# Kernel tuning notes

Measured on AMD Instinct MI355X. Metric: run time of the kernel, lower is better.

The kernel has to match this reference:

```python
import jax, jax.numpy as jnp
import numpy as np

D_MODEL = 384
NUM_CODES = 256
BETAS = (0.05, 0.25, 0.6)
B = 8192


def _vq(x, codebook, beta):
    """Standard EMA-VQ forward: nearest-code lookup + straight-through + commitment loss.
    x: (B, N, D), codebook: (K, D).
    (EMA buffer updates are training-time, no-grad side effects and are omitted.)"""
    flat = x.reshape(-1, x.shape[-1])  # (B*N, D)
    d2 = (jnp.sum(flat * flat, axis=-1, keepdims=True)
          - 2.0 * flat @ codebook.T
          + jnp.sum(codebook * codebook, axis=-1))  # (B*N, K)
    idx = jnp.argmin(d2, axis=-1)                    # (B*N,)
    q_hard = codebook[idx].reshape(x.shape)          # gather (B, N, D)
    idx = idx.reshape(x.shape[:-1])                  # (B, N)
    loss = beta * jnp.mean(jnp.square(jax.lax.stop_gradient(q_hard) - x))
    q = x + jax.lax.stop_gradient(q_hard - x)        # straight-through estimator
    return q, loss, idx


def setup_inputs() -> dict:
    key = jax.random.key(0)
    k0, k1, k2, k3, k4, k5 = jax.random.split(key, 6)
    return {
        "l0_feats": jax.random.normal(k0, (B, 4, D_MODEL), dtype=jnp.float32),
        "l1_feats": jax.random.normal(k1, (B, 16, D_MODEL), dtype=jnp.float32),
        "l2_feats": jax.random.normal(k2, (B, 16, D_MODEL), dtype=jnp.float32),
        "codebook0": jax.random.normal(k3, (NUM_CODES, D_MODEL), dtype=jnp.float32),
        "codebook1": jax.random.normal(k4, (NUM_CODES, D_MODEL), dtype=jnp.float32),
        "codebook2": jax.random.normal(k5, (NUM_CODES, D_MODEL), dtype=jnp.float32),
    }


def reference(l0_feats, l1_feats, l2_feats, codebook0, codebook1, codebook2):
    q0, loss0, idx0 = _vq(l0_feats, codebook0, BETAS[0])
    q1, loss1, idx1 = _vq(l1_feats, codebook1, BETAS[1])
    q2, loss2, idx2 = _vq(l2_feats, codebook2, BETAS[2])
    total_vq_loss = loss0 + loss1 + loss2
    return (idx0, idx1, idx2, total_vq_loss, q0, q1, q2)
```

## Files before the change

kernel.cpp:

```cpp
#include <hip/hip_runtime.h>


typedef _Float16 half8 __attribute__((ext_vector_type(8)));
typedef float f32x16 __attribute__((ext_vector_type(16)));

#define D_MODEL 384
#define NSEG 96
#define NKT 12
#define BM 64
#define RTAU 0.5f

__device__ __forceinline__ float4 ld4(const float* p) { return *(const float4*)p; }

__device__ __forceinline__ half8 cvt8h(const float4& a, const float4& b) {
  half8 h;
  h[0] = (_Float16)a.x; h[1] = (_Float16)a.y; h[2] = (_Float16)a.z; h[3] = (_Float16)a.w;
  h[4] = (_Float16)b.x; h[5] = (_Float16)b.y; h[6] = (_Float16)b.z; h[7] = (_Float16)b.w;
  return h;
}

__device__ __forceinline__ void gload_lds16(const void* g, void* l) {
  __builtin_amdgcn_global_load_lds(
      (const __attribute__((address_space(1))) unsigned int*)g,
      (__attribute__((address_space(3))) unsigned int*)l, 16, 0, 0);
}

__global__ __launch_bounds__(64) void vq_norms(const float* __restrict__ c0,
                                               const float* __restrict__ c1,
                                               const float* __restrict__ c2,
                                               float* __restrict__ en,
                                               int* __restrict__ counts) {
  if (blockIdx.x == 0 && threadIdx.x < 4) counts[threadIdx.x] = 0;
  const int row = blockIdx.x;
  const float* cb = (row < 256) ? c0 : ((row < 512) ? c1 : c2);
  const int n = row & 255;
  const int lane = threadIdx.x;
  const float* r = cb + (size_t)n * D_MODEL;
  float s = 0.f;
  for (int c = lane; c < D_MODEL; c += 64) s = fmaf(r[c], r[c], s);
  for (int m = 1; m < 64; m <<= 1) s += __shfl_xor(s, m, 64);
  if (lane == 0) en[row] = s;
}

__global__ __launch_bounds__(256) void vq_split_cb(const float* __restrict__ c0,
                                                   const float* __restrict__ c1,
                                                   const float* __restrict__ c2,
                                                   half8* __restrict__ bh) {
  const int t = blockIdx.x * 256 + threadIdx.x;
  const int lvl = t / 12288;
  const int rem = t - lvl * 12288;
  const int kt = rem >> 10;
  const int f = (rem >> 6) & 15;
  const int lane = rem & 63;
  const int code = (f >> 1) * 32 + (lane & 31);
  const int k0 = kt * 32 + (f & 1) * 16 + (lane >> 5) * 8;
  const float* cb = (lvl == 0) ? c0 : ((lvl == 1) ? c1 : c2);
  const float4 a = ld4(cb + code * D_MODEL + k0);
  const float4 b = ld4(cb + code * D_MODEL + k0 + 4);
  bh[t] = cvt8h(a, b);
}

__global__ __launch_bounds__(256, 3) void vq_mfma_all(
    const float* __restrict__ l0, const float* __restrict__ l1,
    const float* __restrict__ l2, const float* __restrict__ c0,
    const float* __restrict__ c1, const float* __restrict__ c2,
    const float* __restrict__ en_all,
    const half8* __restrict__ bh_pre,
    float* __restrict__ out, float* __restrict__ dmin_all,
    float* __restrict__ xn_all,
    int* __restrict__ list0, int* __restrict__ list1, int* __restrict__ list2,
    int* __restrict__ counts) {
  __shared__ __align__(16) unsigned char smem[40960];
  float*  scanbuf = (float*)smem;
  float4* red     = (float4*)(smem + 32768);
  float*  en_s    = (float*)(smem + 36864);
  float4* rowres  = (float4*)(smem + 37888);
  float*  xns     = (float*)(smem + 38912);
  int*    idxs    = (int*)(smem + 39168);

  const int swz = (blockIdx.x & 7) * 576 + (blockIdx.x >> 3);
  int lvl, blk;
  if (swz < 512)       { lvl = 0; blk = swz; }
  else if (swz < 2560) { lvl = 1; blk = swz - 512; }
  else                 { lvl = 2; blk = swz - 2560; }
  const float* x  = (lvl == 0) ? l0 : ((lvl == 1) ? l1 : l2);
  const float* cb = (lvl == 0) ? c0 : ((lvl == 1) ? c1 : c2);
  const float* en = en_all + lvl * 256;
  const half8* bh = bh_pre + lvl * 12288;
  const long ioff = (lvl == 0) ? 0 : ((lvl == 1) ? 32768 : 163840);
  float* out_idx = out + ioff;
  float* out_q   = out + ((lvl == 0) ? 294913L : ((lvl == 1) ? 12877825L : 63209473L));
  float* dmin_lvl = dmin_all + ioff;
  float* xn_lvl   = xn_all + ioff;
  int* list = (lvl == 0) ? list0 : ((lvl == 1) ? list1 : list2);
  int* cnt  = counts + lvl;

  const int tid = threadIdx.x;
  const int lane = tid & 63;
  const int w = tid >> 6, wm = w >> 1, wn = w & 1;
  const int c31 = lane & 31, h = lane >> 5;
  const long m0 = (long)blk * BM;

  const float* ap = x + (m0 + wm * 32 + c31) * (long)D_MODEL + h * 8;

  f32x16 acc[4];
#pragma unroll
  for (int n = 0; n < 4; ++n)
#pragma unroll
    for (int i = 0; i < 16; ++i) acc[n][i] = 0.f;

  float xn_part = 0.f;

  float4 ra0 = ld4(ap + 0), ra1 = ld4(ap + 4), ra2 = ld4(ap + 16), ra3 = ld4(ap + 20);
#pragma unroll
  for (int r = 0; r < 4; ++r) {
    const int f = r * 4 + w;
    gload_lds16(bh + (size_t)(f * 64 + lane), (void*)(smem + f * 1024));
  }
  xn_part = fmaf(ra0.x, ra0.x, xn_part); xn_part = fmaf(ra0.y, ra0.y, xn_part);
  xn_part = fmaf(ra0.z, ra0.z, xn_part); xn_part = fmaf(ra0.w, ra0.w, xn_part);
  xn_part = fmaf(ra1.x, ra1.x, xn_part); xn_part = fmaf(ra1.y, ra1.y, xn_part);
  xn_part = fmaf(ra1.z, ra1.z, xn_part); xn_part = fmaf(ra1.w, ra1.w, xn_part);
  xn_part = fmaf(ra2.x, ra2.x, xn_part); xn_part = fmaf(ra2.y, ra2.y, xn_part);
  xn_part = fmaf(ra2.z, ra2.z, xn_part); xn_part = fmaf(ra2.w, ra2.w, xn_part);
  xn_part = fmaf(ra3.x, ra3.x, xn_part); xn_part = fmaf(ra3.y, ra3.y, xn_part);
  xn_part = fmaf(ra3.z, ra3.z, xn_part); xn_part = fmaf(ra3.w, ra3.w, xn_part);
  half8 ahc0 = cvt8h(ra0, ra1);
  half8 ahc1 = cvt8h(ra2, ra3);
  __syncthreads();

#pragma unroll
  for (int kt = 0; kt < NKT; ++kt) {
    const int cur = kt & 1;
    const int nxt = cur ^ 1;
    float4 rb0, rb1, rb2, rb3;
    if (kt + 1 < NKT) {
#pragma unroll
      for (int r = 0; r < 4; ++r) {
        const int f = r * 4 + w;
        gload_lds16(bh + (size_t)(kt + 1) * 1024 + (size_t)(f * 64 + lane),
                    (void*)(smem + nxt * 16384 + f * 1024));
      }
      const int ko = (kt + 1) * 32;
      rb0 = ld4(ap + ko); rb1 = ld4(ap + ko + 4);
      rb2 = ld4(ap + ko + 16); rb3 = ld4(ap + ko + 20);
    }
    {
      const half8* Bh = (const half8*)(smem + cur * 16384);
#pragma unroll
      for (int n = 0; n < 4; ++n) {
        const int nt = wn * 4 + n;
        half8 b0 = Bh[(nt * 2 + 0) * 64 + lane];
        half8 b1 = Bh[(nt * 2 + 1) * 64 + lane];
        acc[n] = __builtin_amdgcn_mfma_f32_32x32x16_f16(ahc0, b0, acc[n], 0, 0, 0);
        acc[n] = __builtin_amdgcn_mfma_f32_32x32x16_f16(ahc1, b1, acc[n], 0, 0, 0);
      }
    }
    if (kt + 1 < NKT) {
      xn_part = fmaf(rb0.x, rb0.x, xn_part); xn_part = fmaf(rb0.y, rb0.y, xn_part);
      xn_part = fmaf(rb0.z, rb0.z, xn_part); xn_part = fmaf(rb0.w, rb0.w, xn_part);
      xn_part = fmaf(rb1.x, rb1.x, xn_part); xn_part = fmaf(rb1.y, rb1.y, xn_part);
      xn_part = fmaf(rb1.z, rb1.z, xn_part); xn_part = fmaf(rb1.w, rb1.w, xn_part);
      xn_part = fmaf(rb2.x, rb2.x, xn_part); xn_part = fmaf(rb2.y, rb2.y, xn_part);
      xn_part = fmaf(rb2.z, rb2.z, xn_part); xn_part = fmaf(rb2.w, rb2.w, xn_part);
      xn_part = fmaf(rb3.x, rb3.x, xn_part); xn_part = fmaf(rb3.y, rb3.y, xn_part);
      xn_part = fmaf(rb3.z, rb3.z, xn_part); xn_part = fmaf(rb3.w, rb3.w, xn_part);
      ahc0 = cvt8h(rb0, rb1);
      ahc1 = cvt8h(rb2, rb3);
      __syncthreads();
    }
  }

  {
    const float xr = xn_part + __shfl_xor(xn_part, 32, 64);
    if (wn == 0 && lane < 32) xns[wm * 32 + lane] = xr;
  }
  en_s[tid] = en[tid];

#pragma unroll 1
  for (int b = 0; b < 2; ++b) {
    __syncthreads();
    if (wm == b) {
#pragma unroll
      for (int n = 0; n < 4; ++n) {
        const int colbase = wn * 128 + n * 32 + c31;
#pragma unroll
        for (int rr = 0; rr < 16; ++rr) {
          const int row_b = (rr & 3) + ((rr >> 2) << 3) + (h << 2);
          const int p = colbase ^ ((row_b & 3) << 3);
          scanbuf[row_b * 256 + p] = fmaf(-2.f, acc[n][rr], en_s[colbase]);
        }
      }
    }
    __syncthreads();
    {
      const int srow = tid >> 3, chunk = tid & 7;
      float b1 = 1e30f, b2 = 1e30f; int i1 = 0, i2 = 0;
#pragma unroll
      for (int u = 0; u < 32; ++u) {
        const int col = chunk + u * 8;
        const float d = scanbuf[srow * 256 + (col ^ ((srow & 3) << 3))];
        if (d < b1) { b2 = b1; i2 = i1; b1 = d; i1 = col; }
        else if (d < b2) { b2 = d; i2 = col; }
      }
      red[srow * 8 + chunk] = make_float4(b1, __int_as_float(i1), b2, __int_as_float(i2));
    }
    __syncthreads();
    if (tid < 32) {
      float4 q = red[tid * 8 + 0];
      float fb1 = q.x, fb2 = q.z;
      int fi1 = __float_as_int(q.y), fi2 = __float_as_int(q.w);
#pragma unroll
      for (int c = 1; c < 8; ++c) {
        q = red[tid * 8 + c];
        const float c1 = q.x, c2 = q.z;
        const int j1 = __float_as_int(q.y), j2 = __float_as_int(q.w);
        if (c1 < fb1 || (c1 == fb1 && j1 < fi1)) {
          if (fb1 < c2 || (fb1 == c2 && fi1 < j2)) { fb2 = fb1; fi2 = fi1; }
          else { fb2 = c2; fi2 = j2; }
          fb1 = c1; fi1 = j1;
        } else if (c1 < fb2 || (c1 == fb2 && j1 < fi2)) { fb2 = c1; fi2 = j1; }
      }
      rowres[b * 32 + tid] = make_float4(fb1, __int_as_float(fi1), fb2, __int_as_float(fi2));
    }
  }
  __syncthreads();

  if (tid < BM) {
    const int m = tid;
    const float4 qv = rowres[m];
    const float fb1 = qv.x, fb2 = qv.z;
    const int fi1 = __float_as_int(qv.y);
    const float xn = xns[m];
    idxs[m] = fi1;
    out_idx[m0 + m] = (float)fi1;
    dmin_lvl[m0 + m] = xn + fb1;
    xn_lvl[m0 + m] = xn;
    const bool flg = (fb2 - fb1 < RTAU);
    const unsigned long long mask = __ballot(flg);
    const int nf = __popcll(mask);
    int base = 0;
    if (tid == 0 && nf) base = atomicAdd(cnt, nf);
    base = __shfl(base, 0, 64);
    if (flg) {
      const int pos = __popcll(mask & ((1ull << tid) - 1ull));
      list[base + pos] = (int)(m0 + m);
    }
  }
  __syncthreads();

  float* qb = out_q + m0 * (long)D_MODEL;
  for (int g = tid; g < BM * NSEG; g += 256) {
    const int m = g / NSEG;
    const int seg = g - m * NSEG;
    *(float4*)(qb + m * (long)D_MODEL + seg * 4) = ld4(cb + (long)idxs[m] * D_MODEL + seg * 4);
  }
}

__global__ __launch_bounds__(256) void vq_rescue_all(
    const float* __restrict__ l0, const float* __restrict__ l1,
    const float* __restrict__ l2, const float* __restrict__ c0,
    const float* __restrict__ c1, const float* __restrict__ c2,
    const float* __restrict__ en_all,
    const int* __restrict__ list0, const int* __restrict__ list1,
    const int* __restrict__ list2, const int* __restrict__ counts,
    float* __restrict__ out, float* __restrict__ dmin_all,
    const float* __restrict__ xn_all) {
  __shared__ float xs[8][D_MODEL];
  __shared__ double dall[8][256];
  __shared__ int rows_s[8];
  __shared__ float xns_s[8];
  __shared__ int best_s[8];

  const int lvl = blockIdx.x >> 7;
  const int sb  = blockIdx.x & 127;
  const float* x  = (lvl == 0) ? l0 : ((lvl == 1) ? l1 : l2);
  const float* cb = (lvl == 0) ? c0 : ((lvl == 1) ? c1 : c2);
  const int* list = (lvl == 0) ? list0 : ((lvl == 1) ? list1 : list2);
  const long ioff = (lvl == 0) ? 0 : ((lvl == 1) ? 32768 : 163840);
  float* out_idx = out + ioff;
  float* out_q   = out + ((lvl == 0) ? 294913L : ((lvl == 1) ? 12877825L : 63209473L));
  float* dmin_lvl = dmin_all + ioff;
  const float* xn_lvl = xn_all + ioff;

  const int tid = threadIdx.x;
  const int count = counts[lvl];
  const int nch = (count + 7) >> 3;
  const int w = tid >> 6, lane = tid & 63;
  const float* crow = cb + (long)tid * D_MODEL;

  for (int c = sb; c < nch; c += 128) {
    const int base = c << 3;
    const int R = min(8, count - base);
    if (tid < 8) {
      const int j = min(tid, R - 1);
      const int r = list[base + j];
      rows_s[tid] = r;
      xns_s[tid] = xn_lvl[r];
    }
    __syncthreads();
#pragma unroll
    for (int r = 0; r < 8; ++r)
      if (tid < NSEG) *(float4*)&xs[r][tid * 4] = ld4(x + (long)rows_s[r] * D_MODEL + tid * 4);
    __syncthreads();

    double en_d = 0.0;
    double dot[8] = {0.0, 0.0, 0.0, 0.0, 0.0, 0.0, 0.0, 0.0};
    for (int k = 0; k < D_MODEL; ++k) {
      const double cd = (double)crow[k];
      en_d = fma(cd, cd, en_d);
#pragma unroll
      for (int r = 0; r < 8; ++r)
        dot[r] = fma(cd, (double)xs[r][k], dot[r]);
    }
#pragma unroll
    for (int r = 0; r < 8; ++r)
      dall[r][tid] = fma(-2.0, dot[r], en_d);
    __syncthreads();

#pragma unroll
    for (int rr = 0; rr < 2; ++rr) {
      const int r = w + rr * 4;
      if (r < R) {
        double best = dall[r][lane]; int bidx = lane;
#pragma unroll
        for (int u = 1; u < 4; ++u) {
          const int code = lane + u * 64;
          const double d = dall[r][code];
          if (d < best) { best = d; bidx = code; }
        }
        for (int mm = 1; mm < 64; mm <<= 1) {
          const double ov = __shfl_xor(best, mm, 64);
          const int oi = __shfl_xor(bidx, mm, 64);
          if (ov < best || (ov == best && oi < bidx)) { best = ov; bidx = oi; }
        }
        if (lane == 0) {
          const int row = rows_s[r];
          out_idx[row] = (float)bidx;
          dmin_lvl[row] = xns_s[r] + (float)best;
          best_s[r] = bidx;
        }
      }
    }
    __syncthreads();
#pragma unroll
    for (int r = 0; r < 8; ++r)
      if (r < R && tid < NSEG)
        *(float4*)(out_q + (long)rows_s[r] * D_MODEL + tid * 4) =
            ld4(cb + (long)best_s[r] * D_MODEL + tid * 4);
    __syncthreads();
  }
}

__global__ __launch_bounds__(256) void loss_stage1(const float* __restrict__ dmin,
                                                   double* __restrict__ lp) {
  const int b = blockIdx.x;
  const int tid = threadIdx.x;
  const long r0 = (long)b * 512;
  __shared__ double sh[256];
  sh[tid] = (double)dmin[r0 + tid] + (double)dmin[r0 + 256 + tid];
  __syncthreads();
  for (int st = 128; st > 0; st >>= 1) {
    if (tid < st) sh[tid] += sh[tid + st];
    __syncthreads();
  }
  if (tid == 0) {
    double scale;
    if (b < 64)       scale = 0.05 / (32768.0 * 384.0);
    else if (b < 320) scale = 0.25 / (131072.0 * 384.0);
    else              scale = 0.60 / (131072.0 * 384.0);
    lp[b] = sh[0] * scale;
  }
}

__global__ __launch_bounds__(256) void loss_stage2(const double* __restrict__ lp,
                                                   float* __restrict__ out_loss) {
  const int tid = threadIdx.x;
  __shared__ double sh[256];
  sh[tid] = lp[tid] + lp[tid + 256] + ((tid < 64) ? lp[tid + 512] : 0.0);
  __syncthreads();
  for (int st = 128; st > 0; st >>= 1) {
    if (tid < st) sh[tid] += sh[tid + st];
    __syncthreads();
  }
  if (tid == 0) out_loss[0] = (float)sh[0];
}

extern "C" void kernel_launch(void* const* d_in, const int* in_sizes, int n_in,
                              void* d_out, int out_size, void* d_ws, size_t ws_size,
                              hipStream_t stream) {
  const float* l0 = (const float*)d_in[0];
  const float* l1 = (const float*)d_in[1];
  const float* l2 = (const float*)d_in[2];
  const float* c0 = (const float*)d_in[3];
  const float* c1 = (const float*)d_in[4];
  const float* c2 = (const float*)d_in[5];
  float* out = (float*)d_out;

  float* wsf = (float*)d_ws;
  int*   counts   = (int*)wsf;
  float* en       = wsf + 4;
  float* dmin_all = wsf + 772;
  float* xn_all   = wsf + 295684;
  int*   list0    = (int*)(wsf + 590596);
  int*   list1    = (int*)(wsf + 623364);
  int*   list2    = (int*)(wsf + 754436);
  double* lp      = (double*)(wsf + 885508);
  half8* bh_pre   = (half8*)(wsf + 886660);

  vq_norms<<<768, 64, 0, stream>>>(c0, c1, c2, en, counts);
  vq_split_cb<<<144, 256, 0, stream>>>(c0, c1, c2, bh_pre);

  vq_mfma_all<<<4608, 256, 0, stream>>>(l0, l1, l2, c0, c1, c2, en,
                                        bh_pre, out,
                                        dmin_all, xn_all,
                                        list0, list1, list2, counts);

  vq_rescue_all<<<384, 256, 0, stream>>>(l0, l1, l2, c0, c1, c2, en,
                                         list0, list1, list2, counts,
                                         out, dmin_all, xn_all);

  loss_stage1<<<576, 256, 0, stream>>>(dmin_all, lp);
  loss_stage2<<<1, 256, 0, stream>>>(lp, out + 294912);
}
```

Baseline: 482.0 us.

## Read codebook fragments from global directly in MFMA loop, widen rescue grid

The MFMA distance kernel no longer stages the pre-split fp16 codebook tiles through LDS with async global-to-LDS loads and per-step barriers. Each wave now loads its B fragments straight from global memory (mostly L2-resident, since the codebook is small) into registers, which removes the double-buffered LDS pipeline and the per-k-tile __syncthreads. The rescue kernel grid grows from 128 to 1024 blocks per level so more chunks of ambiguous rows run in parallel. In exchange, B fragments are loaded redundantly by each wave instead of shared through LDS, and global load latency is exposed in the MFMA loop.

Result: slower. 526.2 us (+9.2%).

```diff
diff --git a/kernel.cpp b/kernel.cpp
--- a/kernel.cpp
+++ b/kernel.cpp
@@ -17,12 +17,6 @@
   h[0] = (_Float16)a.x; h[1] = (_Float16)a.y; h[2] = (_Float16)a.z; h[3] = (_Float16)a.w;
   h[4] = (_Float16)b.x; h[5] = (_Float16)b.y; h[6] = (_Float16)b.z; h[7] = (_Float16)b.w;
   return h;
-}
-
-__device__ __forceinline__ void gload_lds16(const void* g, void* l) {
-  __builtin_amdgcn_global_load_lds(
-      (const __attribute__((address_space(1))) unsigned int*)g,
-      (__attribute__((address_space(3))) unsigned int*)l, 16, 0, 0);
 }
 
 __global__ __launch_bounds__(64) void vq_norms(const float* __restrict__ c0,
@@ -59,6 +53,16 @@
   const float4 b = ld4(cb + code * D_MODEL + k0 + 4);
   bh[t] = cvt8h(a, b);
 }
+
+#define XN8(v0, v1, v2, v3)                                                     \
+  xn_part = fmaf(v0.x, v0.x, xn_part); xn_part = fmaf(v0.y, v0.y, xn_part);     \
+  xn_part = fmaf(v0.z, v0.z, xn_part); xn_part = fmaf(v0.w, v0.w, xn_part);     \
+  xn_part = fmaf(v1.x, v1.x, xn_part); xn_part = fmaf(v1.y, v1.y, xn_part);     \
+  xn_part = fmaf(v1.z, v1.z, xn_part); xn_part = fmaf(v1.w, v1.w, xn_part);     \
+  xn_part = fmaf(v2.x, v2.x, xn_part); xn_part = fmaf(v2.y, v2.y, xn_part);     \
+  xn_part = fmaf(v2.z, v2.z, xn_part); xn_part = fmaf(v2.w, v2.w, xn_part);     \
+  xn_part = fmaf(v3.x, v3.x, xn_part); xn_part = fmaf(v3.y, v3.y, xn_part);     \
+  xn_part = fmaf(v3.z, v3.z, xn_part); xn_part = fmaf(v3.w, v3.w, xn_part);
 
 __global__ __launch_bounds__(256, 3) void vq_mfma_all(
     const float* __restrict__ l0, const float* __restrict__ l1,
@@ -102,6 +106,7 @@
   const long m0 = (long)blk * BM;
 
   const float* ap = x + (m0 + wm * 32 + c31) * (long)D_MODEL + h * 8;
+  const half8* bhw = bh + wn * 512 + lane;
 
   f32x16 acc[4];
 #pragma unroll
@@ -112,62 +117,37 @@
   float xn_part = 0.f;
 
   float4 ra0 = ld4(ap + 0), ra1 = ld4(ap + 4), ra2 = ld4(ap + 16), ra3 = ld4(ap + 20);
-#pragma unroll
-  for (int r = 0; r < 4; ++r) {
-    const int f = r * 4 + w;
-    gload_lds16(bh + (size_t)(f * 64 + lane), (void*)(smem + f * 1024));
-  }
-  xn_part = fmaf(ra0.x, ra0.x, xn_part); xn_part = fmaf(ra0.y, ra0.y, xn_part);
-  xn_part = fmaf(ra0.z, ra0.z, xn_part); xn_part = fmaf(ra0.w, ra0.w, xn_part);
-  xn_part = fmaf(ra1.x, ra1.x, xn_part); xn_part = fmaf(ra1.y, ra1.y, xn_part);
-  xn_part = fmaf(ra1.z, ra1.z, xn_part); xn_part = fmaf(ra1.w, ra1.w, xn_part);
-  xn_part = fmaf(ra2.x, ra2.x, xn_part); xn_part = fmaf(ra2.y, ra2.y, xn_part);
-  xn_part = fmaf(ra2.z, ra2.z, xn_part); xn_part = fmaf(ra2.w, ra2.w, xn_part);
-  xn_part = fmaf(ra3.x, ra3.x, xn_part); xn_part = fmaf(ra3.y, ra3.y, xn_part);
-  xn_part = fmaf(ra3.z, ra3.z, xn_part); xn_part = fmaf(ra3.w, ra3.w, xn_part);
+  XN8(ra0, ra1, ra2, ra3)
   half8 ahc0 = cvt8h(ra0, ra1);
   half8 ahc1 = cvt8h(ra2, ra3);
-  __syncthreads();
 
 #pragma unroll
   for (int kt = 0; kt < NKT; ++kt) {
-    const int cur = kt & 1;
-    const int nxt = cur ^ 1;
-    float4 rb0, rb1, rb2, rb3;
+    half8 b0 = bhw[kt * 1024 + 0 * 64];
+    half8 b1 = bhw[kt * 1024 + 1 * 64];
+    half8 b2 = bhw[kt * 1024 + 2 * 64];
+    half8 b3 = bhw[kt * 1024 + 3 * 64];
+    half8 b4 = bhw[kt * 1024 + 4 * 64];
+    half8 b5 = bhw[kt * 1024 + 5 * 64];
+    half8 b6 = bhw[kt * 1024 + 6 * 64];
+    half8 b7 = bhw[kt * 1024 + 7 * 64];
     if (kt + 1 < NKT) {
-#pragma unroll
-      for (int r = 0; r < 4; ++r) {
-        const int f = r * 4 + w;
-        gload_lds16(bh + (size_t)(kt + 1) * 1024 + (size_t)(f * 64 + lane),
-                    (void*)(smem + nxt * 16384 + f * 1024));
-      }
       const int ko = (kt + 1) * 32;
-      rb0 = ld4(ap + ko); rb1 = ld4(ap + ko + 4);
-      rb2 = ld4(ap + ko + 16); rb3 = ld4(ap + ko + 20);
-    }
-    {
-      const half8* Bh = (const half8*)(smem + cur * 16384);
-#pragma unroll
-      for (int n = 0; n < 4; ++n) {
-        const int nt = wn * 4 + n;
-        half8 b0 = Bh[(nt * 2 + 0) * 64 + lane];
-        half8 b1 = Bh[(nt * 2 + 1) * 64 + lane];
-        acc[n] = __builtin_amdgcn_mfma_f32_32x32x16_f16(ahc0, b0, acc[n], 0, 0, 0);
-        acc[n] = __builtin_amdgcn_mfma_f32_32x32x16_f16(ahc1, b1, acc[n], 0, 0, 0);
-      }
-    }
+      ra0 = ld4(ap + ko);      ra1 = ld4(ap + ko + 4);
+      ra2 = ld4(ap + ko + 16); ra3 = ld4(ap + ko + 20);
+    }
+    acc[0] = __builtin_amdgcn_mfma_f32_32x32x16_f16(ahc0, b0, acc[0], 0, 0, 0);
+    acc[0] = __builtin_amdgcn_mfma_f32_32x32x16_f16(ahc1, b1, acc[0], 0, 0, 0);
+    acc[1] = __builtin_amdgcn_mfma_f32_32x32x16_f16(ahc0, b2, acc[1], 0, 0, 0);
+    acc[1] = __builtin_amdgcn_mfma_f32_32x32x16_f16(ahc1, b3, acc[1], 0, 0, 0);
+    acc[2] = __builtin_amdgcn_mfma_f32_32x32x16_f16(ahc0, b4, acc[2], 0, 0, 0);
+    acc[2] = __builtin_amdgcn_mfma_f32_32x32x16_f16(ahc1, b5, acc[2], 0, 0, 0);
+    acc[3] = __builtin_amdgcn_mfma_f32_32x32x16_f16(ahc0, b6, acc[3], 0, 0, 0);
+    acc[3] = __builtin_amdgcn_mfma_f32_32x32x16_f16(ahc1, b7, acc[3], 0, 0, 0);
     if (kt + 1 < NKT) {
-      xn_part = fmaf(rb0.x, rb0.x, xn_part); xn_part = fmaf(rb0.y, rb0.y, xn_part);
-      xn_part = fmaf(rb0.z, rb0.z, xn_part); xn_part = fmaf(rb0.w, rb0.w, xn_part);
-      xn_part = fmaf(rb1.x, rb1.x, xn_part); xn_part = fmaf(rb1.y, rb1.y, xn_part);
-      xn_part = fmaf(rb1.z, rb1.z, xn_part); xn_part = fmaf(rb1.w, rb1.w, xn_part);
-      xn_part = fmaf(rb2.x, rb2.x, xn_part); xn_part = fmaf(rb2.y, rb2.y, xn_part);
-      xn_part = fmaf(rb2.z, rb2.z, xn_part); xn_part = fmaf(rb2.w, rb2.w, xn_part);
-      xn_part = fmaf(rb3.x, rb3.x, xn_part); xn_part = fmaf(rb3.y, rb3.y, xn_part);
-      xn_part = fmaf(rb3.z, rb3.z, xn_part); xn_part = fmaf(rb3.w, rb3.w, xn_part);
-      ahc0 = cvt8h(rb0, rb1);
-      ahc1 = cvt8h(rb2, rb3);
-      __syncthreads();
+      XN8(ra0, ra1, ra2, ra3)
+      ahc0 = cvt8h(ra0, ra1);
+      ahc1 = cvt8h(ra2, ra3);
     }
   }
 
@@ -272,8 +252,8 @@
   __shared__ float xns_s[8];
   __shared__ int best_s[8];
 
-  const int lvl = blockIdx.x >> 7;
-  const int sb  = blockIdx.x & 127;
+  const int lvl = blockIdx.x >> 10;
+  const int sb  = blockIdx.x & 1023;
   const float* x  = (lvl == 0) ? l0 : ((lvl == 1) ? l1 : l2);
   const float* cb = (lvl == 0) ? c0 : ((lvl == 1) ? c1 : c2);
   const int* list = (lvl == 0) ? list0 : ((lvl == 1) ? list1 : list2);
@@ -289,7 +269,7 @@
   const int w = tid >> 6, lane = tid & 63;
   const float* crow = cb + (long)tid * D_MODEL;
 
-  for (int c = sb; c < nch; c += 128) {
+  for (int c = sb; c < nch; c += 1024) {
     const int base = c << 3;
     const int R = min(8, count - base);
     if (tid < 8) {
@@ -416,9 +396,9 @@
                                         dmin_all, xn_all,
                                         list0, list1, list2, counts);
 
-  vq_rescue_all<<<384, 256, 0, stream>>>(l0, l1, l2, c0, c1, c2, en,
-                                         list0, list1, list2, counts,
-                                         out, dmin_all, xn_all);
+  vq_rescue_all<<<3072, 256, 0, stream>>>(l0, l1, l2, c0, c1, c2, en,
+                                          list0, list1, list2, counts,
+                                          out, dmin_all, xn_all);
 
   loss_stage1<<<576, 256, 0, stream>>>(dmin_all, lp);
   loss_stage2<<<1, 256, 0, stream>>>(lp, out + 294912);
```
